# Kernel tuning notes

Hardware: AMD Instinct MI355X
Metric: run time of the kernel (lower is better)

The kernel has to match this reference:

```python
import jax, jax.numpy as jnp
import numpy as np

N, DIN, D, K0, NC = 32768, 768, 512, 128, 2
KS = [128, 64, 32, 16]  # prototype counts per stage (num_protos // 2**i)
NEG_SLOPE = 0.01


def _lin(x, W, b):
    # torch nn.Linear: W is [out, in]
    return x @ W.T + b


def _ln(x, g, b):
    m = x.mean(-1, keepdims=True)
    v = ((x - m) ** 2).mean(-1, keepdims=True)
    return (x - m) * jax.lax.rsqrt(v + 1e-5) * g + b


def setup_inputs() -> dict:
    key = jax.random.key(0)
    ks = jax.random.split(key, 40)
    s = 0.02

    def nrm(k, shp, sc=s):
        return jax.random.normal(k, shp, jnp.float32) * sc

    inp = {}
    inp["data"] = jax.random.normal(ks[0], (N, DIN), jnp.float32)
    inp["prototypes"] = jax.random.normal(ks[1], (K0, DIN), jnp.float32)
    inp["W_pp"] = nrm(ks[2], (D, DIN)); inp["b_pp"] = jnp.zeros((D,), jnp.float32)
    inp["W_cp"] = nrm(ks[3], (D, DIN)); inp["b_cp"] = jnp.zeros((D,), jnp.float32)
    inp["sim_scale"] = jnp.ones((1,), jnp.float32)
    # 3 enhancer MLPs + layernorms (stacked, same shapes)
    inp["enh_w1"] = nrm(ks[4], (3, D, D)); inp["enh_b1"] = jnp.zeros((3, D), jnp.float32)
    inp["enh_w2"] = nrm(ks[5], (3, D, D)); inp["enh_b2"] = jnp.zeros((3, D), jnp.float32)
    inp["ln_g"] = jnp.ones((3, D), jnp.float32); inp["ln_b"] = jnp.zeros((3, D), jnp.float32)
    # ProtoReducers: Mlp along K axis; fc1 [inK,inK], fc2 [outK,inK]
    ki = 6
    for i in range(3):
        inK, outK = KS[i], KS[i + 1]
        inp[f"red_w1_{i}"] = nrm(ks[ki], (inK, inK)); ki += 1
        inp[f"red_b1_{i}"] = jnp.zeros((inK,), jnp.float32)
        inp[f"red_w2_{i}"] = nrm(ks[ki], (outK, inK)); ki += 1
        inp[f"red_b2_{i}"] = jnp.zeros((outK,), jnp.float32)
    inp["W_proc"] = nrm(ks[20], (D, D)); inp["b_proc"] = jnp.zeros((D,), jnp.float32)
    inp["g_an"] = jnp.ones((D,), jnp.float32); inp["b_an"] = jnp.zeros((D,), jnp.float32)
    inp["W_t"] = nrm(ks[21], (D, D)); inp["b_t"] = jnp.zeros((D,), jnp.float32)
    inp["W_g"] = nrm(ks[22], (D, D)); inp["b_g"] = jnp.zeros((D,), jnp.float32)
    inp["W_s"] = nrm(ks[23], (1, D)); inp["b_s"] = jnp.zeros((1,), jnp.float32)
    inp["W_h"] = nrm(ks[24], (D, D)); inp["b_h"] = jnp.zeros((D,), jnp.float32)
    inp["W_c"] = nrm(ks[25], (NC, D)); inp["b_c"] = jnp.zeros((NC,), jnp.float32)
    return inp


def reference(data, prototypes, W_pp, b_pp, W_cp, b_cp, sim_scale,
              enh_w1, enh_b1, enh_w2, enh_b2, ln_g, ln_b,
              red_w1_0, red_b1_0, red_w2_0, red_b2_0,
              red_w1_1, red_b1_1, red_w2_1, red_b2_1,
              red_w1_2, red_b1_2, red_w2_2, red_b2_2,
              W_proc, b_proc, g_an, b_an,
              W_t, b_t, W_g, b_g, W_s, b_s, W_h, b_h, W_c, b_c):
    # patch / prototype projections (Linear + LeakyReLU)
    P = jax.nn.leaky_relu(_lin(data, W_pp, b_pp), NEG_SLOPE)        # [N, D]
    C = jax.nn.leaky_relu(_lin(prototypes, W_cp, b_cp), NEG_SLOPE)  # [K0, D]
    # denom = max(1e-6, tau * similarity_scale.item()); tau=1, no grad through scale
    denom = jnp.maximum(1e-6, jax.lax.stop_gradient(sim_scale)[0])
    reds = [(red_w1_0, red_b1_0, red_w2_0, red_b2_0),
            (red_w1_1, red_b1_1, red_w2_1, red_b2_1),
            (red_w1_2, red_b1_2, red_w2_2, red_b2_2)]
    for i in range(3):
        # L2 similarity: -cdist(P, C) computed as a GEMM
        d2 = (jnp.sum(P * P, -1, keepdims=True) + jnp.sum(C * C, -1)[None, :]
              - 2.0 * (P @ C.T))
        sim = -jnp.sqrt(jnp.maximum(d2, 1e-12))                     # [N, K]
        A = jax.nn.softmax(sim / denom, axis=1)                     # soft routing
        ctx = A @ C                                                 # [N, D]
        P = _ln(P + ctx, ln_g[i], ln_b[i])
        P = P + _lin(jax.nn.relu(_lin(P, enh_w1[i], enh_b1[i])), enh_w2[i], enh_b2[i])
        # ProtoReducer: Mlp over K axis (operate on C.T of shape [D, K])
        w1, b1, w2, b2 = reds[i]
        Ct = _lin(jax.nn.relu(_lin(C.T, w1, b1)), w2, b2)           # [D, Kout]
        C = Ct.T
    Z = jnp.concatenate([P, C], axis=0)                             # [N+16, D]
    Z = jax.nn.relu(_lin(Z, W_proc, b_proc))
    Z = _ln(Z, g_an, b_an)
    # gated attention MIL pooling
    t = jnp.tanh(_lin(Z, W_t, b_t))
    g = jax.nn.sigmoid(_lin(Z, W_g, b_g))
    scores = _lin(t * g, W_s, b_s)                                  # [N+16, 1]
    Aw = jax.nn.softmax(scores, axis=0)
    bag = Aw.T @ Z                                                  # [1, D]
    h = jax.nn.relu(_lin(bag, W_h, b_h))
    logits = _lin(h, W_c, b_c)                                      # [1, 2]
    return logits
```

## Files before the change

kernel.cpp:

```cpp
#include <hip/hip_runtime.h>
#include <math.h>

typedef _Float16 f16x8 __attribute__((ext_vector_type(8)));
typedef _Float16 f16x4 __attribute__((ext_vector_type(4)));
typedef float f32x4 __attribute__((ext_vector_type(4)));

#define TBM 256
#define TBN 128
#define TBK 32

#define AS1 __attribute__((address_space(1)))
#define AS3 __attribute__((address_space(3)))

__device__ __forceinline__ void gll16(const _Float16* g, _Float16* l)
{
    __builtin_amdgcn_global_load_lds((const AS1 unsigned int*)g,
                                     (AS3 unsigned int*)l, 16, 0, 0);
}

__device__ __forceinline__ int xcd_swz(int bid, int nwg)
{
    if ((nwg & 7) == 0) {
        int chunk = nwg >> 3;
        bid = (bid & 7) * chunk + (bid >> 3);
    }
    return bid;
}

__device__ __forceinline__ float fsigmoid(float x)
{
    return __builtin_amdgcn_rcpf(1.f + __expf(-x));
}
__device__ __forceinline__ float ftanh(float x)
{
    float ax = fabsf(x);
    float e = __expf(-2.f * ax);
    float t = (1.f - e) * __builtin_amdgcn_rcpf(1.f + e);
    return copysignf(t, x);
}

template<int ACT, bool F16OUT>
__global__ __launch_bounds__(256)
void dot_k(const float* __restrict__ X, const float* __restrict__ W,
           const float* __restrict__ bias, void* __restrict__ Yv,
           int M, int K)
{
    int gw = (blockIdx.x * 256 + threadIdx.x) >> 6;
    int lane = threadIdx.x & 63;
    if (gw >= M * 512) return;
    int r = gw >> 9, n = gw & 511;
    const float* xr = X + (size_t)r * K;
    const float* wr = W + (size_t)n * K;
    float d = 0.f;
    for (int t = 0; t < K; t += 256) {
        float4 a = *(const float4*)(xr + t + lane * 4);
        float4 b = *(const float4*)(wr + t + lane * 4);
        d += a.x * b.x + a.y * b.y + a.z * b.z + a.w * b.w;
    }
#pragma unroll
    for (int o = 32; o; o >>= 1) d += __shfl_xor(d, o);
    if (lane == 0) {
        float v = d + bias[n];
        if (ACT == 1) v = v > 0.f ? v : 0.01f * v;
        else if (ACT == 2) v = fmaxf(v, 0.f);
        if (F16OUT) ((_Float16*)Yv)[(size_t)r * 512 + n] = (_Float16)v;
        else        ((float*)Yv)[(size_t)r * 512 + n] = v;
    }
}

template<int MODE, int ACT, bool F32OUT>
__global__ __launch_bounds__(512)
void mgemm(const _Float16* __restrict__ A, const _Float16* __restrict__ B,
           const float* __restrict__ bias, _Float16* __restrict__ Yh,
           float* __restrict__ Yf, int M, int K, int Nout)
{
    __shared__ _Float16 As[2][TBM * TBK];
    __shared__ _Float16 Bs[2][TBN * TBK];
    const int tid = threadIdx.x;
    const int lane = tid & 63;
    const int wid = tid >> 6;
    const int wr = wid >> 1, wc = wid & 1;

    int bid = xcd_swz(blockIdx.y * gridDim.x + blockIdx.x, gridDim.x * gridDim.y);
    const int m0 = (bid / gridDim.x) * TBM;
    const int n0 = (bid % gridDim.x) * TBN;

    f32x4 acc[4][4] = {};
    const int nt = K / TBK;

    const int lrow = lane >> 2;
    const int lk = (lane & 3) * 8;

    auto stage = [&](int t, int buf) {
        const int k0 = t * TBK;
#pragma unroll
        for (int q = 0; q < 2; q++) {
            int c = wid * 2 + q;
            int r = c * 16 + lrow;
            int am = min(m0 + r, M - 1);
            gll16(A + (size_t)am * K + k0 + lk, &As[buf][c * 512]);
        }
        {
            int c = wid;
            int r = c * 16 + lrow;
            int bn = min(n0 + r, Nout - 1);
            gll16(B + (size_t)bn * K + k0 + lk, &Bs[buf][c * 512]);
        }
    };

    stage(0, 0);
    __syncthreads();
    for (int t = 0; t < nt; ++t) {
        const int cur = t & 1;
        if (t + 1 < nt) stage(t + 1, cur ^ 1);
        f16x8 af[4], bf[4];
#pragma unroll
        for (int mi = 0; mi < 4; mi++)
            af[mi] = *(const f16x8*)(&As[cur][(wr * 64 + mi * 16 + (lane & 15)) * TBK + (lane >> 4) * 8]);
#pragma unroll
        for (int nj = 0; nj < 4; nj++)
            bf[nj] = *(const f16x8*)(&Bs[cur][(wc * 64 + nj * 16 + (lane & 15)) * TBK + (lane >> 4) * 8]);
#pragma unroll
        for (int mi = 0; mi < 4; mi++)
#pragma unroll
            for (int nj = 0; nj < 4; nj++)
                acc[mi][nj] = __builtin_amdgcn_mfma_f32_16x16x32_f16(af[mi], bf[nj], acc[mi][nj], 0, 0, 0);
        __syncthreads();
    }

#pragma unroll
    for (int mi = 0; mi < 4; mi++) {
        int mbase = m0 + wr * 64 + mi * 16 + (lane >> 4) * 4;
#pragma unroll
        for (int nj = 0; nj < 4; nj++) {
            int n = n0 + wc * 64 + nj * 16 + (lane & 15);
            if (n < Nout) {
                float bv = bias ? bias[n] : 0.f;
#pragma unroll
                for (int r = 0; r < 4; r++) {
                    int m = mbase + r;
                    if (m < M) {
                        float v = acc[mi][nj][r] + bv;
                        size_t idx = (size_t)m * Nout + n;
                        if (MODE == 0) {
                            if (ACT == 1) v = v > 0.f ? v : 0.01f * v;
                            else if (ACT == 2) v = fmaxf(v, 0.f);
                            if (F32OUT) Yf[idx] = v;
                            else        Yh[idx] = (_Float16)v;
                        } else {
                            float s = (float)Yh[idx] + v;
                            Yh[idx] = (_Float16)s;
                        }
                    }
                }
            }
        }
    }
}

__global__ __launch_bounds__(512)
void gatgemm(const _Float16* __restrict__ A, const _Float16* __restrict__ B1,
             const _Float16* __restrict__ B2, const float* __restrict__ c1,
             const float* __restrict__ c2, _Float16* __restrict__ Y,
             int M, int K, int Nout)
{
    __shared__ _Float16 As[2][TBM * TBK];
    __shared__ _Float16 B1s[2][TBN * TBK];
    __shared__ _Float16 B2s[2][TBN * TBK];
    const int tid = threadIdx.x;
    const int lane = tid & 63;
    const int wid = tid >> 6;
    const int wr = wid >> 1, wc = wid & 1;

    int bid = xcd_swz(blockIdx.y * gridDim.x + blockIdx.x, gridDim.x * gridDim.y);
    const int m0 = (bid / gridDim.x) * TBM;
    const int n0 = (bid % gridDim.x) * TBN;

    f32x4 acc1[4][4] = {};
    f32x4 acc2[4][4] = {};
    const int nt = K / TBK;

    const int lrow = lane >> 2;
    const int lk = (lane & 3) * 8;

    auto stage = [&](int t, int buf) {
        const int k0 = t * TBK;
#pragma unroll
        for (int q = 0; q < 2; q++) {
            int c = wid * 2 + q;
            int r = c * 16 + lrow;
            int am = min(m0 + r, M - 1);
            gll16(A + (size_t)am * K + k0 + lk, &As[buf][c * 512]);
        }
        {
            int c = wid;
            int r = c * 16 + lrow;
            int bn = min(n0 + r, Nout - 1);
            gll16(B1 + (size_t)bn * K + k0 + lk, &B1s[buf][c * 512]);
            gll16(B2 + (size_t)bn * K + k0 + lk, &B2s[buf][c * 512]);
        }
    };

    stage(0, 0);
    __syncthreads();
    for (int t = 0; t < nt; ++t) {
        const int cur = t & 1;
        if (t + 1 < nt) stage(t + 1, cur ^ 1);
        f16x8 af[4], bf1[4], bf2[4];
#pragma unroll
        for (int mi = 0; mi < 4; mi++)
            af[mi] = *(const f16x8*)(&As[cur][(wr * 64 + mi * 16 + (lane & 15)) * TBK + (lane >> 4) * 8]);
#pragma unroll
        for (int nj = 0; nj < 4; nj++) {
            int ro = (wc * 64 + nj * 16 + (lane & 15)) * TBK + (lane >> 4) * 8;
            bf1[nj] = *(const f16x8*)(&B1s[cur][ro]);
            bf2[nj] = *(const f16x8*)(&B2s[cur][ro]);
        }
#pragma unroll
        for (int mi = 0; mi < 4; mi++)
#pragma unroll
            for (int nj = 0; nj < 4; nj++) {
                acc1[mi][nj] = __builtin_amdgcn_mfma_f32_16x16x32_f16(af[mi], bf1[nj], acc1[mi][nj], 0, 0, 0);
                acc2[mi][nj] = __builtin_amdgcn_mfma_f32_16x16x32_f16(af[mi], bf2[nj], acc2[mi][nj], 0, 0, 0);
            }
        __syncthreads();
    }

#pragma unroll
    for (int mi = 0; mi < 4; mi++) {
        int mbase = m0 + wr * 64 + mi * 16 + (lane >> 4) * 4;
#pragma unroll
        for (int nj = 0; nj < 4; nj++) {
            int n = n0 + wc * 64 + nj * 16 + (lane & 15);
            if (n < Nout) {
                float bv1 = c1[n], bv2 = c2[n];
#pragma unroll
                for (int r = 0; r < 4; r++) {
                    int m = mbase + r;
                    if (m < M) {
                        float t1 = ftanh(acc1[mi][nj][r] + bv1);
                        float g1 = fsigmoid(acc2[mi][nj][r] + bv2);
                        Y[(size_t)m * Nout + n] = (_Float16)(t1 * g1);
                    }
                }
            }
        }
    }
}

#define SBM 128
__global__ __launch_bounds__(256)
void simgemm(const _Float16* __restrict__ A, const _Float16* __restrict__ B,
             const float* __restrict__ Psq, const float* __restrict__ Csq,
             const float* __restrict__ sscale, _Float16* __restrict__ Ah,
             int M, int K, int Kin)
{
    __shared__ _Float16 As[2][SBM * TBK];
    __shared__ _Float16 Bs[2][SBM * TBK];
    __shared__ float redmx[2][SBM];
    __shared__ float redsm[2][SBM];
    const int tid = threadIdx.x;
    const int lane = tid & 63;
    const int wid = tid >> 6;
    const int wr = wid >> 1, wc = wid & 1;
    const int m0 = blockIdx.y * SBM;

    f32x4 acc[4][4] = {};
    const int nt = K / TBK;
    const int lrow = lane >> 2;
    const int lk = (lane & 3) * 8;

    auto stage = [&](int t, int buf) {
        const int k0 = t * TBK;
#pragma unroll
        for (int q = 0; q < 2; q++) {
            int c = wid * 2 + q;
            int r = c * 16 + lrow;
            int am = min(m0 + r, M - 1);
            int bn = min(r, Kin - 1);
            gll16(A + (size_t)am * K + k0 + lk, &As[buf][c * 512]);
            gll16(B + (size_t)bn * K + k0 + lk, &Bs[buf][c * 512]);
        }
    };

    stage(0, 0);
    __syncthreads();
    for (int t = 0; t < nt; ++t) {
        const int cur = t & 1;
        if (t + 1 < nt) stage(t + 1, cur ^ 1);
        f16x8 af[4], bf[4];
#pragma unroll
        for (int mi = 0; mi < 4; mi++)
            af[mi] = *(const f16x8*)(&As[cur][(wr * 64 + mi * 16 + (lane & 15)) * TBK + (lane >> 4) * 8]);
#pragma unroll
        for (int nj = 0; nj < 4; nj++)
            bf[nj] = *(const f16x8*)(&Bs[cur][(wc * 64 + nj * 16 + (lane & 15)) * TBK + (lane >> 4) * 8]);
#pragma unroll
        for (int mi = 0; mi < 4; mi++)
#pragma unroll
            for (int nj = 0; nj < 4; nj++)
                acc[mi][nj] = __builtin_amdgcn_mfma_f32_16x16x32_f16(af[mi], bf[nj], acc[mi][nj], 0, 0, 0);
        __syncthreads();
    }

    const float denom = fmaxf(1e-6f, sscale[0]);
    const int colbase = wc * 64 + (lane & 15);
    const int g = lane >> 4;
    float cc[4];
#pragma unroll
    for (int nj = 0; nj < 4; nj++) {
        int n = colbase + nj * 16;
        cc[nj] = (n < Kin) ? Csq[n] : 0.f;
    }

#pragma unroll
    for (int mi = 0; mi < 4; mi++) {
#pragma unroll
        for (int r = 0; r < 4; r++) {
            int row = wr * 64 + mi * 16 + g * 4 + r;
            float pp = Psq[m0 + row];
            float mx = -INFINITY;
#pragma unroll
            for (int nj = 0; nj < 4; nj++) {
                int n = colbase + nj * 16;
                float v = -INFINITY;
                if (n < Kin)
                    v = -sqrtf(fmaxf(pp + cc[nj] - 2.f * acc[mi][nj][r], 1e-12f)) / denom;
                acc[mi][nj][r] = v;
                mx = fmaxf(mx, v);
            }
#pragma unroll
            for (int o = 1; o < 16; o <<= 1) mx = fmaxf(mx, __shfl_xor(mx, o));
            if ((lane & 15) == 0) redmx[wc][row] = mx;
        }
    }
    __syncthreads();

#pragma unroll
    for (int mi = 0; mi < 4; mi++) {
#pragma unroll
        for (int r = 0; r < 4; r++) {
            int row = wr * 64 + mi * 16 + g * 4 + r;
            float mx = fmaxf(redmx[0][row], redmx[1][row]);
            float s = 0.f;
#pragma unroll
            for (int nj = 0; nj < 4; nj++) {
                int n = colbase + nj * 16;
                float e = (n < Kin) ? __expf(acc[mi][nj][r] - mx) : 0.f;
                acc[mi][nj][r] = e;
                s += e;
            }
#pragma unroll
            for (int o = 1; o < 16; o <<= 1) s += __shfl_xor(s, o);
            if ((lane & 15) == 0) redsm[wc][row] = s;
        }
    }
    __syncthreads();

#pragma unroll
    for (int mi = 0; mi < 4; mi++) {
#pragma unroll
        for (int r = 0; r < 4; r++) {
            int row = wr * 64 + mi * 16 + g * 4 + r;
            float inv = __builtin_amdgcn_rcpf(redsm[0][row] + redsm[1][row]);
            int m = m0 + row;
#pragma unroll
            for (int nj = 0; nj < 4; nj++) {
                int n = colbase + nj * 16;
                if (n < Kin)
                    Ah[(size_t)m * Kin + n] = (_Float16)(acc[mi][nj][r] * inv);
            }
        }
    }
}

__global__ __launch_bounds__(256)
void cvt_k(const float* __restrict__ x, _Float16* __restrict__ y, int n)
{
    int i = (blockIdx.x * 256 + threadIdx.x) * 4;
    if (i < n) {
        float4 v = *(const float4*)(x + i);
        f16x4 h = { (_Float16)v.x, (_Float16)v.y, (_Float16)v.z, (_Float16)v.w };
        *(f16x4*)(y + i) = h;
    }
}

__global__ __launch_bounds__(256)
void cvtC_k(const float* __restrict__ C, _Float16* __restrict__ Ch,
            _Float16* __restrict__ CTh, int Kin)
{
    int i = blockIdx.x * 256 + threadIdx.x;
    if (i < Kin * 512) {
        int j = i >> 9, d = i & 511;
        float v = C[i];
        Ch[i] = (_Float16)v;
        CTh[d * Kin + j] = (_Float16)v;
    }
}

__global__ __launch_bounds__(256)
void rowsq_k(const _Float16* __restrict__ X, float* __restrict__ out, int M)
{
    int wid = threadIdx.x >> 6, lane = threadIdx.x & 63;
    int row = blockIdx.x * 4 + wid;
    if (row >= M) return;
    f16x8 a = *(const f16x8*)(X + (size_t)row * 512 + lane * 8);
    float s = 0.f;
#pragma unroll
    for (int q = 0; q < 8; q++) { float f = (float)a[q]; s += f * f; }
#pragma unroll
    for (int o = 32; o; o >>= 1) s += __shfl_xor(s, o);
    if (lane == 0) out[row] = s;
}

__global__ __launch_bounds__(256)
void ln_k(const _Float16* __restrict__ X, const _Float16* __restrict__ R,
          const float* __restrict__ g, const float* __restrict__ b,
          _Float16* __restrict__ Yh, int M)
{
    int wid = threadIdx.x >> 6, lane = threadIdx.x & 63;
    int row = blockIdx.x * 4 + wid;
    if (row >= M) return;
    f16x8 a = *(const f16x8*)(X + (size_t)row * 512 + lane * 8);
    float v[8];
#pragma unroll
    for (int q = 0; q < 8; q++) v[q] = (float)a[q];
    if (R) {
        f16x8 c = *(const f16x8*)(R + (size_t)row * 512 + lane * 8);
#pragma unroll
        for (int q = 0; q < 8; q++) v[q] += (float)c[q];
    }
    float s = 0.f, ss = 0.f;
#pragma unroll
    for (int q = 0; q < 8; q++) { s += v[q]; ss += v[q] * v[q]; }
#pragma unroll
    for (int o = 32; o; o >>= 1) { s += __shfl_xor(s, o); ss += __shfl_xor(ss, o); }
    float mean = s * (1.f / 512.f);
    float var = ss * (1.f / 512.f) - mean * mean;
    float inv = 1.f / sqrtf(var + 1e-5f);
    int d0 = lane * 8;
    f16x8 o8;
#pragma unroll
    for (int q = 0; q < 8; q++)
        o8[q] = (_Float16)((v[q] - mean) * inv * g[d0 + q] + b[d0 + q]);
    *(f16x8*)(Yh + (size_t)row * 512 + d0) = o8;
}

__global__ __launch_bounds__(256)
void red1_k(const float* __restrict__ C, const float* __restrict__ w1,
            const float* __restrict__ b1, float* __restrict__ H1, int Kin)
{
    int d = blockIdx.x * 256 + threadIdx.x;
    int j = blockIdx.y;
    float acc = b1[j];
    for (int k = 0; k < Kin; k++) acc = fmaf(C[(size_t)k * 512 + d], w1[(size_t)j * Kin + k], acc);
    H1[(size_t)j * 512 + d] = fmaxf(acc, 0.f);
}

__global__ __launch_bounds__(256)
void red2_k(const float* __restrict__ H1, const float* __restrict__ w2,
            const float* __restrict__ b2, float* __restrict__ Cn, int Kin, int Kout)
{
    int d = blockIdx.x * 256 + threadIdx.x;
    int j2 = blockIdx.y;
    float acc = b2[j2];
    for (int j = 0; j < Kin; j++) acc = fmaf(H1[(size_t)j * 512 + d], w2[(size_t)j2 * Kin + j], acc);
    Cn[(size_t)j2 * 512 + d] = acc;
}

__global__ __launch_bounds__(256)
void score_k(const _Float16* __restrict__ TG, const float* __restrict__ Ws,
             const float* __restrict__ bs, float* __restrict__ out, int M)
{
    int wid = threadIdx.x >> 6, lane = threadIdx.x & 63;
    int row = blockIdx.x * 4 + wid;
    if (row >= M) return;
    f16x8 a = *(const f16x8*)(TG + (size_t)row * 512 + lane * 8);
    float4 w0 = *(const float4*)(Ws + lane * 8);
    float4 w1 = *(const float4*)(Ws + lane * 8 + 4);
    float d = (float)a[0] * w0.x + (float)a[1] * w0.y + (float)a[2] * w0.z + (float)a[3] * w0.w
            + (float)a[4] * w1.x + (float)a[5] * w1.y + (float)a[6] * w1.z + (float)a[7] * w1.w;
#pragma unroll
    for (int o = 32; o; o >>= 1) d += __shfl_xor(d, o);
    if (lane == 0) out[row] = d + bs[0];
}

__global__ __launch_bounds__(1024)
void pool_k(float* __restrict__ s, float* __restrict__ scal, int M)
{
    __shared__ float sm[16];
    int tid = threadIdx.x, lane = tid & 63, wid = tid >> 6;
    float mx = -INFINITY;
    for (int i = tid * 4; i < M; i += 4096) {
        float4 a = *(const float4*)(s + i);
        mx = fmaxf(fmaxf(fmaxf(mx, a.x), fmaxf(a.y, a.z)), a.w);
    }
#pragma unroll
    for (int o = 32; o; o >>= 1) mx = fmaxf(mx, __shfl_xor(mx, o));
    if (lane == 0) sm[wid] = mx;
    __syncthreads();
    if (wid == 0) {
        float v = (lane < 16) ? sm[lane] : -INFINITY;
#pragma unroll
        for (int o = 8; o; o >>= 1) v = fmaxf(v, __shfl_xor(v, o));
        if (lane == 0) sm[0] = v;
    }
    __syncthreads();
    float gmax = sm[0];
    __syncthreads();
    float sum = 0.f;
    for (int i = tid * 4; i < M; i += 4096) {
        float4 a = *(const float4*)(s + i);
        float4 e;
        e.x = __expf(a.x - gmax); e.y = __expf(a.y - gmax);
        e.z = __expf(a.z - gmax); e.w = __expf(a.w - gmax);
        *(float4*)(s + i) = e;
        sum += e.x + e.y + e.z + e.w;
    }
#pragma unroll
    for (int o = 32; o; o >>= 1) sum += __shfl_xor(sum, o);
    if (lane == 0) sm[wid] = sum;
    __syncthreads();
    if (tid == 0) {
        float t = 0.f;
        for (int w = 0; w < 16; w++) t += sm[w];
        scal[0] = t;
    }
}

__global__ __launch_bounds__(256)
void bagp_k(const _Float16* __restrict__ Z, const float* __restrict__ w,
            float* __restrict__ PB, int M, int cs)
{
    int d = blockIdx.x * 256 + threadIdx.x;
    int chunk = blockIdx.y;
    int i0 = chunk * cs;
    int i1 = min(M, i0 + cs);
    float acc = 0.f;
    for (int i = i0; i < i1; i++) acc = fmaf(w[i], (float)Z[(size_t)i * 512 + d], acc);
    PB[(size_t)chunk * 512 + d] = acc;
}

__global__ __launch_bounds__(256)
void bagf_k(const float* __restrict__ PB, const float* __restrict__ scal,
            float* __restrict__ bag, int nchunk)
{
    int d = blockIdx.x * 256 + threadIdx.x;
    float acc = 0.f;
    for (int c = 0; c < nchunk; c++) acc += PB[(size_t)c * 512 + d];
    bag[d] = acc / scal[0];
}

__global__ __launch_bounds__(256)
void h_k(const float* __restrict__ bag, const float* __restrict__ Wh,
         const float* __restrict__ bh, float* __restrict__ h)
{
    int wid = threadIdx.x >> 6, lane = threadIdx.x & 63;
    int j = blockIdx.x * 4 + wid;
    const float* wr = Wh + (size_t)j * 512;
    float d = 0.f;
#pragma unroll
    for (int t = 0; t < 2; t++) {
        float4 a = *(const float4*)(wr + t * 256 + lane * 4);
        float4 bv = *(const float4*)(bag + t * 256 + lane * 4);
        d += a.x * bv.x + a.y * bv.y + a.z * bv.z + a.w * bv.w;
    }
#pragma unroll
    for (int o = 32; o; o >>= 1) d += __shfl_xor(d, o);
    if (lane == 0) h[j] = fmaxf(d + bh[j], 0.f);
}

__global__ __launch_bounds__(128)
void logit_k(const float* __restrict__ h, const float* __restrict__ Wc,
             const float* __restrict__ bc, float* __restrict__ out)
{
    int wid = threadIdx.x >> 6, lane = threadIdx.x & 63;
    const float* wr = Wc + (size_t)wid * 512;
    float d = 0.f;
#pragma unroll
    for (int t = 0; t < 2; t++) {
        float4 a = *(const float4*)(wr + t * 256 + lane * 4);
        float4 hv = *(const float4*)(h + t * 256 + lane * 4);
        d += a.x * hv.x + a.y * hv.y + a.z * hv.z + a.w * hv.w;
    }
#pragma unroll
    for (int o = 32; o; o >>= 1) d += __shfl_xor(d, o);
    if (lane == 0) out[wid] = d + bc[wid];
}

extern "C" void kernel_launch(void* const* d_in, const int* in_sizes, int n_in,
                              void* d_out, int out_size, void* d_ws, size_t ws_size,
                              hipStream_t stream)
{
    const float* data    = (const float*)d_in[0];
    const float* protos  = (const float*)d_in[1];
    const float* W_pp    = (const float*)d_in[2];
    const float* b_pp    = (const float*)d_in[3];
    const float* W_cp    = (const float*)d_in[4];
    const float* b_cp    = (const float*)d_in[5];
    const float* sscale  = (const float*)d_in[6];
    const float* enh_w1  = (const float*)d_in[7];
    const float* enh_b1  = (const float*)d_in[8];
    const float* enh_w2  = (const float*)d_in[9];
    const float* enh_b2  = (const float*)d_in[10];
    const float* ln_g    = (const float*)d_in[11];
    const float* ln_b    = (const float*)d_in[12];
    const float* red_w1[3] = {(const float*)d_in[13], (const float*)d_in[17], (const float*)d_in[21]};
    const float* red_b1[3] = {(const float*)d_in[14], (const float*)d_in[18], (const float*)d_in[22]};
    const float* red_w2[3] = {(const float*)d_in[15], (const float*)d_in[19], (const float*)d_in[23]};
    const float* red_b2[3] = {(const float*)d_in[16], (const float*)d_in[20], (const float*)d_in[24]};
    const float* W_proc  = (const float*)d_in[25];
    const float* b_proc  = (const float*)d_in[26];
    const float* g_an    = (const float*)d_in[27];
    const float* b_an    = (const float*)d_in[28];
    const float* W_t     = (const float*)d_in[29];
    const float* b_t     = (const float*)d_in[30];
    const float* W_g     = (const float*)d_in[31];
    const float* b_g     = (const float*)d_in[32];
    const float* W_s     = (const float*)d_in[33];
    const float* b_s     = (const float*)d_in[34];
    const float* W_h     = (const float*)d_in[35];
    const float* b_h     = (const float*)d_in[36];
    const float* W_c     = (const float*)d_in[37];
    const float* b_c     = (const float*)d_in[38];
    float* out = (float*)d_out;

    constexpr int N = 32768, DIN = 768, D = 512;
    constexpr int NCHUNK = 256;
    char* w = (char*)d_ws;
    auto alloc = [&](size_t bytes) -> char* {
        char* p = w; w += (bytes + 255) & ~(size_t)255; return p;
    };
    _Float16* Ph     = (_Float16*)alloc((size_t)N * D * 2);
    _Float16* CTXh   = (_Float16*)alloc((size_t)N * D * 2);
    _Float16* TMPh   = (_Float16*)alloc((size_t)N * D * 2);
    _Float16* Zrawh  = (_Float16*)alloc((size_t)(N + 16) * D * 2);
    _Float16* Zh     = (_Float16*)alloc((size_t)(N + 16) * D * 2);
    _Float16* TGh    = (_Float16*)alloc((size_t)(N + 16) * D * 2);
    _Float16* datah  = (_Float16*)alloc((size_t)N * DIN * 2);
    _Float16* Ah     = (_Float16*)alloc((size_t)N * 128 * 2);
    _Float16* Ch     = (_Float16*)alloc(128 * D * 2);
    _Float16* CTh    = (_Float16*)alloc(128 * D * 2);
    _Float16* Wpph   = (_Float16*)alloc((size_t)D * DIN * 2);
    _Float16* w1h    = (_Float16*)alloc((size_t)3 * D * D * 2);
    _Float16* w2h    = (_Float16*)alloc((size_t)3 * D * D * 2);
    _Float16* Wproch = (_Float16*)alloc((size_t)D * D * 2);
    _Float16* Wth    = (_Float16*)alloc((size_t)D * D * 2);
    _Float16* Wgh    = (_Float16*)alloc((size_t)D * D * 2);
    float*    Psq    = (float*)alloc((size_t)N * 4);
    float*    Csq    = (float*)alloc(128 * 4);
    float*    Ca     = (float*)alloc(128 * D * 4);
    float*    Cb     = (float*)alloc(128 * D * 4);
    float*    H1     = (float*)alloc(128 * D * 4);
    float*    scr    = (float*)alloc((size_t)(N + 16) * 4);
    float*    PB     = (float*)alloc((size_t)NCHUNK * D * 4);
    float*    bag    = (float*)alloc(D * 4);
    float*    hb     = (float*)alloc(D * 4);
    float*    scal   = (float*)alloc(8 * 4);

    dim3 blk(256);
    dim3 blk512(512);
    auto cgrid = [](size_t n) { return dim3((unsigned)((n / 4 + 255) / 256)); };
    auto mgrid = [](int M_, int Nout_) { return dim3((Nout_ + TBN - 1) / TBN, (M_ + TBM - 1) / TBM); };

    cvt_k<<<cgrid((size_t)N * DIN), blk, 0, stream>>>(data, datah, N * DIN);
    cvt_k<<<cgrid((size_t)D * DIN), blk, 0, stream>>>(W_pp, Wpph, D * DIN);
    cvt_k<<<cgrid((size_t)3 * D * D), blk, 0, stream>>>(enh_w1, w1h, 3 * D * D);
    cvt_k<<<cgrid((size_t)3 * D * D), blk, 0, stream>>>(enh_w2, w2h, 3 * D * D);
    cvt_k<<<cgrid((size_t)D * D), blk, 0, stream>>>(W_proc, Wproch, D * D);
    cvt_k<<<cgrid((size_t)D * D), blk, 0, stream>>>(W_t, Wth, D * D);
    cvt_k<<<cgrid((size_t)D * D), blk, 0, stream>>>(W_g, Wgh, D * D);

    mgemm<0, 1, false><<<mgrid(N, D), blk512, 0, stream>>>(datah, Wpph, b_pp, Ph, nullptr, N, DIN, D);
    dot_k<1, false><<<dim3(128 * 512 / 4), blk, 0, stream>>>(protos, W_cp, b_cp, Ca, 128, DIN);

    float* C = Ca;
    float* Cn = Cb;
    int Kin = 128;
    for (int i = 0; i < 3; i++) {
        int Kout = Kin >> 1;
        rowsq_k<<<dim3((N + 3) / 4), blk, 0, stream>>>(Ph, Psq, N);
        cvtC_k<<<dim3((Kin * D + 255) / 256), blk, 0, stream>>>(C, Ch, CTh, Kin);
        rowsq_k<<<dim3((Kin + 3) / 4), blk, 0, stream>>>(Ch, Csq, Kin);
        simgemm<<<dim3(1, N / SBM), blk, 0, stream>>>(Ph, Ch, Psq, Csq, sscale, Ah, N, D, Kin);
        mgemm<0, 0, false><<<mgrid(N, D), blk512, 0, stream>>>(Ah, CTh, nullptr, CTXh, nullptr, N, Kin, D);
        ln_k<<<dim3((N + 3) / 4), blk, 0, stream>>>(Ph, CTXh, ln_g + (size_t)i * D, ln_b + (size_t)i * D, Ph, N);
        mgemm<0, 2, false><<<mgrid(N, D), blk512, 0, stream>>>(Ph, w1h + (size_t)i * D * D, enh_b1 + (size_t)i * D, TMPh, nullptr, N, D, D);
        mgemm<1, 0, false><<<mgrid(N, D), blk512, 0, stream>>>(TMPh, w2h + (size_t)i * D * D, enh_b2 + (size_t)i * D, Ph, nullptr, N, D, D);
        red1_k<<<dim3(2, Kin), blk, 0, stream>>>(C, red_w1[i], red_b1[i], H1, Kin);
        red2_k<<<dim3(2, Kout), blk, 0, stream>>>(H1, red_w2[i], red_b2[i], Cn, Kin, Kout);
        float* t = C; C = Cn; Cn = t;
        Kin = Kout;
    }

    mgemm<0, 2, false><<<mgrid(N, D), blk512, 0, stream>>>(Ph, Wproch, b_proc, Zrawh, nullptr, N, D, D);
    dot_k<2, true><<<dim3(16 * 512 / 4), blk, 0, stream>>>(C, W_proc, b_proc, Zrawh + (size_t)N * D, 16, D);
    ln_k<<<dim3((N + 16 + 3) / 4), blk, 0, stream>>>(Zrawh, nullptr, g_an, b_an, Zh, N + 16);

    gatgemm<<<mgrid(N + 16, D), blk512, 0, stream>>>(Zh, Wth, Wgh, b_t, b_g, TGh, N + 16, D, D);

    score_k<<<dim3((N + 16 + 3) / 4), blk, 0, stream>>>(TGh, W_s, b_s, scr, N + 16);
    pool_k<<<dim3(1), dim3(1024), 0, stream>>>(scr, scal, N + 16);
    int cs = (N + 16 + NCHUNK - 1) / NCHUNK;
    bagp_k<<<dim3(2, NCHUNK), blk, 0, stream>>>(Zh, scr, PB, N + 16, cs);
    bagf_k<<<dim3(2), blk, 0, stream>>>(PB, scal, bag, NCHUNK);

    h_k<<<dim3(128), blk, 0, stream>>>(bag, W_h, b_h, hb);
    logit_k<<<dim3(1), dim3(128), 0, stream>>>(hb, W_c, b_c, out);
}
```

Baseline: 884.8 us.

## Stage GEMM epilogues through LDS for vector stores and fuse row-norm computation

The mgemm and gatgemm epilogues now write accumulator tiles into shared memory in two halves and then store 16-byte vectorized rows to global memory, replacing scattered 2-byte stores. The residual-add mode reads and writes vector chunks the same way. mgemm can also accumulate per-row squared norms into Psq with atomics, which removes the separate rowsq_k pass over P. The C conversion, transpose and norm kernels are merged into one. The cost is extra LDS traffic and barriers in the epilogue, atomic adds, and memsets to clear Psq.

```diff
diff --git a/kernel.cpp b/kernel.cpp
--- a/kernel.cpp
+++ b/kernel.cpp
@@ -68,11 +68,11 @@
     }
 }
 
-template<int MODE, int ACT, bool F32OUT>
+template<int MODE, int ACT, bool SQ>
 __global__ __launch_bounds__(512)
 void mgemm(const _Float16* __restrict__ A, const _Float16* __restrict__ B,
            const float* __restrict__ bias, _Float16* __restrict__ Yh,
-           float* __restrict__ Yf, int M, int K, int Nout)
+           float* __restrict__ Psq, int M, int K, int Nout)
 {
     __shared__ _Float16 As[2][TBM * TBK];
     __shared__ _Float16 Bs[2][TBN * TBK];
@@ -128,32 +128,65 @@
         __syncthreads();
     }
 
-#pragma unroll
-    for (int mi = 0; mi < 4; mi++) {
-        int mbase = m0 + wr * 64 + mi * 16 + (lane >> 4) * 4;
-#pragma unroll
-        for (int nj = 0; nj < 4; nj++) {
-            int n = n0 + wc * 64 + nj * 16 + (lane & 15);
-            if (n < Nout) {
-                float bv = bias ? bias[n] : 0.f;
-#pragma unroll
-                for (int r = 0; r < 4; r++) {
-                    int m = mbase + r;
-                    if (m < M) {
+    _Float16* eb = &As[0][0];
+    const int g = lane >> 4;
+#pragma unroll
+    for (int p = 0; p < 2; p++) {
+        if (p) __syncthreads();
+        if ((wr >> 1) == p) {
+#pragma unroll
+            for (int nj = 0; nj < 4; nj++) {
+                int col = wc * 64 + nj * 16 + (lane & 15);
+                float bv = bias ? bias[n0 + col] : 0.f;
+#pragma unroll
+                for (int mi = 0; mi < 4; mi++)
+#pragma unroll
+                    for (int r = 0; r < 4; r++) {
+                        int lr = (wr & 1) * 64 + mi * 16 + g * 4 + r;
                         float v = acc[mi][nj][r] + bv;
-                        size_t idx = (size_t)m * Nout + n;
                         if (MODE == 0) {
                             if (ACT == 1) v = v > 0.f ? v : 0.01f * v;
                             else if (ACT == 2) v = fmaxf(v, 0.f);
-                            if (F32OUT) Yf[idx] = v;
-                            else        Yh[idx] = (_Float16)v;
-                        } else {
-                            float s = (float)Yh[idx] + v;
-                            Yh[idx] = (_Float16)s;
                         }
+                        eb[lr * 128 + col] = (_Float16)v;
                     }
+            }
+        }
+        __syncthreads();
+        int t4 = tid * 4;
+        int lr = t4 >> 4;
+        int cbase = (t4 & 15) * 8;
+        int m = m0 + p * 128 + lr;
+        float sq = 0.f;
+        if (m < M) {
+#pragma unroll
+            for (int q = 0; q < 4; q++) {
+                int c0 = cbase + q * 8;
+                f16x8 hv = *(f16x8*)(eb + lr * 128 + c0);
+                size_t gidx = (size_t)m * Nout + n0 + c0;
+                if (MODE == 1) {
+                    f16x8 old = *(f16x8*)(Yh + gidx);
+                    f16x8 nw;
+#pragma unroll
+                    for (int e = 0; e < 8; e++) {
+                        float s = (float)old[e] + (float)hv[e];
+                        nw[e] = (_Float16)s;
+                    }
+                    *(f16x8*)(Yh + gidx) = nw;
+                    hv = nw;
+                } else {
+                    *(f16x8*)(Yh + gidx) = hv;
+                }
+                if (SQ) {
+#pragma unroll
+                    for (int e = 0; e < 8; e++) { float f = (float)hv[e]; sq += f * f; }
                 }
             }
+        }
+        if (SQ) {
+            sq += __shfl_xor(sq, 1);
+            sq += __shfl_xor(sq, 2);
+            if ((lane & 3) == 0 && m < M) atomicAdd(&Psq[m], sq);
         }
     }
 }
@@ -226,23 +259,38 @@
         __syncthreads();
     }
 
-#pragma unroll
-    for (int mi = 0; mi < 4; mi++) {
-        int mbase = m0 + wr * 64 + mi * 16 + (lane >> 4) * 4;
-#pragma unroll
-        for (int nj = 0; nj < 4; nj++) {
-            int n = n0 + wc * 64 + nj * 16 + (lane & 15);
-            if (n < Nout) {
-                float bv1 = c1[n], bv2 = c2[n];
-#pragma unroll
-                for (int r = 0; r < 4; r++) {
-                    int m = mbase + r;
-                    if (m < M) {
+    _Float16* eb = &As[0][0];
+    const int g = lane >> 4;
+#pragma unroll
+    for (int p = 0; p < 2; p++) {
+        if (p) __syncthreads();
+        if ((wr >> 1) == p) {
+#pragma unroll
+            for (int nj = 0; nj < 4; nj++) {
+                int col = wc * 64 + nj * 16 + (lane & 15);
+                float bv1 = c1[n0 + col], bv2 = c2[n0 + col];
+#pragma unroll
+                for (int mi = 0; mi < 4; mi++)
+#pragma unroll
+                    for (int r = 0; r < 4; r++) {
+                        int lr = (wr & 1) * 64 + mi * 16 + g * 4 + r;
                         float t1 = ftanh(acc1[mi][nj][r] + bv1);
                         float g1 = fsigmoid(acc2[mi][nj][r] + bv2);
-                        Y[(size_t)m * Nout + n] = (_Float16)(t1 * g1);
+                        eb[lr * 128 + col] = (_Float16)(t1 * g1);
                     }
-                }
+            }
+        }
+        __syncthreads();
+        int t4 = tid * 4;
+        int lr = t4 >> 4;
+        int cbase = (t4 & 15) * 8;
+        int m = m0 + p * 128 + lr;
+        if (m < M) {
+#pragma unroll
+            for (int q = 0; q < 4; q++) {
+                int c0 = cbase + q * 8;
+                f16x8 hv = *(f16x8*)(eb + lr * 128 + c0);
+                *(f16x8*)(Y + (size_t)m * Nout + n0 + c0) = hv;
             }
         }
     }
@@ -386,31 +434,28 @@
 }
 
 __global__ __launch_bounds__(256)
-void cvtC_k(const float* __restrict__ C, _Float16* __restrict__ Ch,
-            _Float16* __restrict__ CTh, int Kin)
-{
-    int i = blockIdx.x * 256 + threadIdx.x;
-    if (i < Kin * 512) {
-        int j = i >> 9, d = i & 511;
-        float v = C[i];
-        Ch[i] = (_Float16)v;
-        CTh[d * Kin + j] = (_Float16)v;
-    }
-}
-
-__global__ __launch_bounds__(256)
-void rowsq_k(const _Float16* __restrict__ X, float* __restrict__ out, int M)
-{
-    int wid = threadIdx.x >> 6, lane = threadIdx.x & 63;
-    int row = blockIdx.x * 4 + wid;
-    if (row >= M) return;
-    f16x8 a = *(const f16x8*)(X + (size_t)row * 512 + lane * 8);
+void cvtC2_k(const float* __restrict__ C, _Float16* __restrict__ Ch,
+             _Float16* __restrict__ CTh, float* __restrict__ Csq, int Kin)
+{
+    int w = threadIdx.x >> 6, lane = threadIdx.x & 63;
+    int row = blockIdx.x * 4 + w;
+    if (row >= Kin) return;
+    float4 a = *(const float4*)(C + (size_t)row * 512 + lane * 8);
+    float4 b = *(const float4*)(C + (size_t)row * 512 + lane * 8 + 4);
+    f16x8 h;
+    h[0] = (_Float16)a.x; h[1] = (_Float16)a.y; h[2] = (_Float16)a.z; h[3] = (_Float16)a.w;
+    h[4] = (_Float16)b.x; h[5] = (_Float16)b.y; h[6] = (_Float16)b.z; h[7] = (_Float16)b.w;
+    *(f16x8*)(Ch + (size_t)row * 512 + lane * 8) = h;
     float s = 0.f;
 #pragma unroll
-    for (int q = 0; q < 8; q++) { float f = (float)a[q]; s += f * f; }
+    for (int q = 0; q < 8; q++) {
+        float f = (float)h[q];
+        s += f * f;
+        CTh[(size_t)(lane * 8 + q) * Kin + row] = h[q];
+    }
 #pragma unroll
     for (int o = 32; o; o >>= 1) s += __shfl_xor(s, o);
-    if (lane == 0) out[row] = s;
+    if (lane == 0) Csq[row] = s;
 }
 
 __global__ __launch_bounds__(256)
@@ -671,7 +716,8 @@
     cvt_k<<<cgrid((size_t)D * D), blk, 0, stream>>>(W_t, Wth, D * D);
     cvt_k<<<cgrid((size_t)D * D), blk, 0, stream>>>(W_g, Wgh, D * D);
 
-    mgemm<0, 1, false><<<mgrid(N, D), blk512, 0, stream>>>(datah, Wpph, b_pp, Ph, nullptr, N, DIN, D);
+    hipMemsetAsync(Psq, 0, (size_t)N * 4, stream);
+    mgemm<0, 1, true><<<mgrid(N, D), blk512, 0, stream>>>(datah, Wpph, b_pp, Ph, Psq, N, DIN, D);
     dot_k<1, false><<<dim3(128 * 512 / 4), blk, 0, stream>>>(protos, W_cp, b_cp, Ca, 128, DIN);
 
     float* C = Ca;
@@ -679,14 +725,16 @@
     int Kin = 128;
     for (int i = 0; i < 3; i++) {
         int Kout = Kin >> 1;
-        rowsq_k<<<dim3((N + 3) / 4), blk, 0, stream>>>(Ph, Psq, N);
-        cvtC_k<<<dim3((Kin * D + 255) / 256), blk, 0, stream>>>(C, Ch, CTh, Kin);
-        rowsq_k<<<dim3((Kin + 3) / 4), blk, 0, stream>>>(Ch, Csq, Kin);
+        cvtC2_k<<<dim3((Kin + 3) / 4), blk, 0, stream>>>(C, Ch, CTh, Csq, Kin);
         simgemm<<<dim3(1, N / SBM), blk, 0, stream>>>(Ph, Ch, Psq, Csq, sscale, Ah, N, D, Kin);
+        if (i < 2) hipMemsetAsync(Psq, 0, (size_t)N * 4, stream);
         mgemm<0, 0, false><<<mgrid(N, D), blk512, 0, stream>>>(Ah, CTh, nullptr, CTXh, nullptr, N, Kin, D);
         ln_k<<<dim3((N + 3) / 4), blk, 0, stream>>>(Ph, CTXh, ln_g + (size_t)i * D, ln_b + (size_t)i * D, Ph, N);
         mgemm<0, 2, false><<<mgrid(N, D), blk512, 0, stream>>>(Ph, w1h + (size_t)i * D * D, enh_b1 + (size_t)i * D, TMPh, nullptr, N, D, D);
-        mgemm<1, 0, false><<<mgrid(N, D), blk512, 0, stream>>>(TMPh, w2h + (size_t)i * D * D, enh_b2 + (size_t)i * D, Ph, nullptr, N, D, D);
+        if (i < 2)
+            mgemm<1, 0, true><<<mgrid(N, D), blk512, 0, stream>>>(TMPh, w2h + (size_t)i * D * D, enh_b2 + (size_t)i * D, Ph, Psq, N, D, D);
+        else
+            mgemm<1, 0, false><<<mgrid(N, D), blk512, 0, stream>>>(TMPh, w2h + (size_t)i * D * D, enh_b2 + (size_t)i * D, Ph, nullptr, N, D, D);
         red1_k<<<dim3(2, Kin), blk, 0, stream>>>(C, red_w1[i], red_b1[i], H1, Kin);
         red2_k<<<dim3(2, Kout), blk, 0, stream>>>(H1, red_w2[i], red_b2[i], Cn, Kin, Kout);
         float* t = C; C = Cn; Cn = t;
```

New measurement: 864.5 us. 2.3% less time.
